# Performance work log

Measured on AMD Instinct MI355X. Metric: run time of the kernel, lower is better.

The kernel has to match this reference:

```python
import jax, jax.numpy as jnp
import numpy as np

ALPHA = 1.0

def setup_inputs() -> dict:
    key = jax.random.key(0)
    k1, k2 = jax.random.split(key)
    N, K, D = 524288, 256, 256
    context = jax.random.normal(k1, (N, D), dtype=jnp.float32)
    clusters = jax.random.normal(k2, (K, D), dtype=jnp.float32)
    return {"context": context, "clusters": clusters}

def reference(context, clusters):
    # Squared euclidean distance via the matmul trick: same math as
    # sum((x[:,None]-c)**2, -1) but avoids materializing (N,K,D).
    x2 = jnp.sum(context * context, axis=1, keepdims=True)          # (N,1)
    c2 = jnp.sum(clusters * clusters, axis=1)                       # (K,)
    xc = context @ clusters.T                                       # (N,K)
    distance = x2 + c2 - 2.0 * xc                                   # (N,K)
    q = 1.0 / (1.0 + distance / ALPHA)
    q = q ** ((ALPHA + 1.0) / 2.0)
    q = q / jnp.sum(q, axis=1, keepdims=True)                        # row-normalize
    return q
```

## Files before the change

kernel.cpp:

```cpp
#include <hip/hip_runtime.h>
#include <hip/hip_bf16.h>


#define DD 256
#define KC 256
#define BM 64
#define NT 2

typedef __attribute__((ext_vector_type(4)))  float f32x4;
typedef __attribute__((ext_vector_type(16))) float f32x16;
typedef __attribute__((ext_vector_type(8)))  short bf16x8;
typedef __attribute__((ext_vector_type(4)))  short bf16x4;
typedef __attribute__((ext_vector_type(4)))  unsigned u32x4;

__device__ __forceinline__ short f2bf(float f) {
    union { float f; unsigned u; } v; v.f = f;
    unsigned r = (v.u + 0x7fffu + ((v.u >> 16) & 1u)) >> 16;
    return (short)r;
}

__device__ __forceinline__ float bf2f(short h) {
    return __builtin_bit_cast(float, ((unsigned)(unsigned short)h) << 16);
}

__device__ __forceinline__ unsigned cvtpk(float a, float b) {
    unsigned r;
    asm("v_cvt_pk_bf16_f32 %0, %1, %2" : "=v"(r) : "v"(a), "v"(b));
    return r;
}

__device__ __forceinline__ float frcp(float x) {
    return __builtin_amdgcn_rcpf(x);
}

template<int CTRL>
__device__ __forceinline__ float dpp_add(float v) {
    int iv = __builtin_bit_cast(int, v);
    int mv = __builtin_amdgcn_update_dpp(0, iv, CTRL, 0xf, 0xf, false);
    return v + __builtin_bit_cast(float, mv);
}
#define QUAD_SWAP1 0xB1

__device__ __forceinline__ f32x4 ld4(const float* p) { return *(const f32x4*)p; }

__global__ __launch_bounds__(64)
void prep_clusters(const float* __restrict__ clus, short* __restrict__ wsb) {
    const int c = blockIdx.x;
    const int t = threadIdx.x;
    f32x4 v = *(const f32x4*)(clus + c * DD + t * 4);
    bf16x4 o;
    o[0] = f2bf(-2.f * v[0]); o[1] = f2bf(-2.f * v[1]);
    o[2] = f2bf(-2.f * v[2]); o[3] = f2bf(-2.f * v[3]);

    const int j    = t >> 1;
    const int ks   = j >> 1;
    const int hi   = j & 1;
    const int half = t & 1;
    const int nj   = c >> 5;
    const int l31  = c & 31;
    *(bf16x4*)&wsb[(((nj * 17 + ks) * 64 + hi * 32 + l31) << 3) + half * 4] = o;

    float s = v[0]*v[0] + v[1]*v[1] + v[2]*v[2] + v[3]*v[3];
    s += __shfl_xor(s, 1);  s += __shfl_xor(s, 2);  s += __shfl_xor(s, 4);
    s += __shfl_xor(s, 8);  s += __shfl_xor(s, 16); s += __shfl_xor(s, 32);
    if (t == 0) {
        float e = 1.f + s;
        short h = f2bf(e);  float e1 = e - bf2f(h);
        short m = f2bf(e1); float e2 = e1 - bf2f(m);
        short l = f2bf(e2);
        u32x4 a;
        a[0] = (unsigned)(unsigned short)h | ((unsigned)(unsigned short)m << 16);
        a[1] = (unsigned)(unsigned short)l;
        a[2] = 0u; a[3] = 0u;
        *(u32x4*)&wsb[((nj * 17 + 16) * 64 + l31) * 8] = a;
        u32x4 z = {0u, 0u, 0u, 0u};
        *(u32x4*)&wsb[((nj * 17 + 16) * 64 + 32 + l31) * 8] = z;
    }
}

__device__ __forceinline__ void convert_tile(const f32x4* u, short* AfB,
                                             float (*x2p)[64], int w, int lane) {
    const int r0   = lane >> 1;
    const int half = lane & 1;
#pragma unroll
    for (int m = 0; m < 2; ++m) {
        float xs = 0.f;
#pragma unroll
        for (int c = 0; c < 2; ++c) {
            f32x4 a0 = u[m * 4 + 2 * c], a1 = u[m * 4 + 2 * c + 1];
            u32x4 o;
            o[0] = cvtpk(a0[0], a0[1]);
            o[1] = cvtpk(a0[2], a0[3]);
            o[2] = cvtpk(a1[0], a1[1]);
            o[3] = cvtpk(a1[2], a1[3]);
            xs += a0[0]*a0[0] + a0[1]*a0[1] + a0[2]*a0[2] + a0[3]*a0[3]
                + a1[0]*a1[0] + a1[1]*a1[1] + a1[2]*a1[2] + a1[3]*a1[3];
            const int j = w * 4 + half * 2 + c;
            *(u32x4*)&AfB[(j * 64 + m * 32 + r0) * 8] = o;
        }
        xs = dpp_add<QUAD_SWAP1>(xs);
        if (half == 0) x2p[w][m * 32 + r0] = xs;
    }
}

__global__ __launch_bounds__(512, 4)
void cluster_q_main(const float* __restrict__ ctx,
                    const short* __restrict__ wsb,
                    float* __restrict__ out) {
    __shared__ short Af[NT][32 * 64 * 8];
    __shared__ float x2p8[NT][8][64];
    __shared__ float rowsum2[8][2][64];

    const int t    = threadIdx.x;
    const int lane = t & 63;
    const int w    = t >> 6;
    const int l31  = lane & 31;
    const int hi   = lane >> 5;
    const size_t row_blk = (size_t)blockIdx.x * (BM * NT);

    const int r0   = lane >> 1;
    const int half = lane & 1;
    const float* src0 = ctx + (row_blk + (size_t)r0) * DD + w * 32 + half * 16;

    f32x4 u[8];

#pragma unroll
    for (int jj = 0; jj < 8; ++jj)
        u[jj] = ld4(src0 + (size_t)((jj >> 2) * 32) * DD + (jj & 3) * 4);
    convert_tile(u, &Af[0][0], x2p8[0], w, lane);
    __syncthreads();

    const short* bl = wsb + (size_t)(w * 17) * 512 + lane * 8;

    bf16x8 ctx_aug = (bf16x8)0;
    if (hi == 0) {
        ctx_aug[0] = (short)0x3F80; ctx_aug[1] = (short)0x3F80;
        ctx_aug[2] = (short)0x3F80;
    }

#pragma unroll
    for (int tile = 0; tile < NT; ++tile) {
        const size_t trow = row_blk + (size_t)tile * BM;

        float x2A = 0.f, x2B = 0.f;
#pragma unroll
        for (int q = 0; q < 8; ++q) {
            x2A += x2p8[tile][q][l31];
            x2B += x2p8[tile][q][32 + l31];
        }

        f32x16 acc0 = (f32x16)0.f, acc1 = (f32x16)0.f;

        bf16x8 bs[3];
        bs[0] = *(const bf16x8*)(bl + 0 * 512);
        bs[1] = *(const bf16x8*)(bl + 1 * 512);
        bf16x8 bsa = *(const bf16x8*)(bl + 16 * 512);

        const short* AfC = &Af[tile][0];
        bf16x8 afA0 = *(const bf16x8*)&AfC[((0 + hi) * 64 +  0 + l31) * 8];
        bf16x8 afA1 = *(const bf16x8*)&AfC[((0 + hi) * 64 + 32 + l31) * 8];
        bf16x8 afB0, afB1;

#pragma unroll
        for (int ks = 0; ks < 16; ++ks) {
            const int cur = ks % 3;
            const bool even = (ks & 1) == 0;

            if (ks < 14)
                bs[(ks + 2) % 3] = *(const bf16x8*)(bl + (ks + 2) * 512);
            if (ks < 15) {
                const int jn = (ks + 1) * 2 + hi;
                bf16x8 v0 = *(const bf16x8*)&AfC[(jn * 64 +  0 + l31) * 8];
                bf16x8 v1 = *(const bf16x8*)&AfC[(jn * 64 + 32 + l31) * 8];
                if (even) { afB0 = v0; afB1 = v1; }
                else      { afA0 = v0; afA1 = v1; }
            }
            if (tile + 1 < NT && (ks & 3) == 0) {
                const int j0 = (ks >> 2) * 2;
#pragma unroll
                for (int jj = 0; jj < 2; ++jj) {
                    const int jx = j0 + jj;
                    u[jx] = ld4(src0 + (size_t)(BM + (jx >> 2) * 32) * DD
                                     + (jx & 3) * 4);
                }
            }

            const bf16x8 a0 = even ? afA0 : afB0;
            const bf16x8 a1 = even ? afA1 : afB1;
            acc0 = __builtin_amdgcn_mfma_f32_32x32x16_bf16(bs[cur], a0, acc0, 0, 0, 0);
            acc1 = __builtin_amdgcn_mfma_f32_32x32x16_bf16(bs[cur], a1, acc1, 0, 0, 0);
        }

        acc0 = __builtin_amdgcn_mfma_f32_32x32x16_bf16(bsa, ctx_aug, acc0, 0, 0, 0);
        acc1 = __builtin_amdgcn_mfma_f32_32x32x16_bf16(bsa, ctx_aug, acc1, 0, 0, 0);

        float s0 = 0.f, s1 = 0.f;
#pragma unroll
        for (int r = 0; r < 16; ++r) {
            acc0[r] = frcp(acc0[r] + x2A); s0 += acc0[r];
            acc1[r] = frcp(acc1[r] + x2B); s1 += acc1[r];
        }
        rowsum2[w][hi][l31]      = s0;
        rowsum2[w][hi][32 + l31] = s1;
        __syncthreads();

        float t0 = 0.f, t1 = 0.f;
#pragma unroll
        for (int q = 0; q < 8; ++q) {
            t0 += rowsum2[q][0][l31]      + rowsum2[q][1][l31];
            t1 += rowsum2[q][0][32 + l31] + rowsum2[q][1][32 + l31];
        }
        const float inv0 = frcp(t0);
        const float inv1 = frcp(t1);

        float* op0 = out + (trow + (size_t)l31) * KC        + w * 32 + 4 * hi;
        float* op1 = out + (trow + (size_t)(32 + l31)) * KC + w * 32 + 4 * hi;
#pragma unroll
        for (int i = 0; i < 4; ++i) {
            f32x4 v0, v1;
#pragma unroll
            for (int j = 0; j < 4; ++j) {
                v0[j] = acc0[4 * i + j] * inv0;
                v1[j] = acc1[4 * i + j] * inv1;
            }
            *(f32x4*)(op0 + 8 * i) = v0;
            *(f32x4*)(op1 + 8 * i) = v1;
        }

        if (tile + 1 < NT) {
            convert_tile(u, &Af[tile + 1][0], x2p8[tile + 1], w, lane);
            __syncthreads();
        }
    }
}

extern "C" void kernel_launch(void* const* d_in, const int* in_sizes, int n_in,
                              void* d_out, int out_size, void* d_ws, size_t ws_size,
                              hipStream_t stream) {
    const float* ctx  = (const float*)d_in[0];
    const float* clus = (const float*)d_in[1];
    float* out = (float*)d_out;

    short* wsb = (short*)d_ws;

    const int nrows = in_sizes[0] / DD;
    const int grid  = nrows / (BM * NT);

    hipLaunchKernelGGL(prep_clusters, dim3(KC), dim3(64), 0, stream, clus, wsb);
    hipLaunchKernelGGL(cluster_q_main, dim3(grid), dim3(512), 0, stream,
                       ctx, wsb, out);
}
```

Measured before the change: 251.4 us.

## Stream K-chunks of a single 64-row tile through double-buffered LDS

Each block now handles one 64-row tile instead of two. The tile's context is loaded in four 64-wide K chunks into a two-slot LDS buffer, and the next chunk is converted while MFMAs run on the current one. This shrinks LDS use, and launch bounds rise to allow 6 blocks per CU, aiming for more occupancy and overlap of global loads with compute. The cost is extra __syncthreads per K chunk and a grid twice as large.

```diff
diff --git a/kernel.cpp b/kernel.cpp
--- a/kernel.cpp
+++ b/kernel.cpp
@@ -5,7 +5,6 @@
 #define DD 256
 #define KC 256
 #define BM 64
-#define NT 2
 
 typedef __attribute__((ext_vector_type(4)))  float f32x4;
 typedef __attribute__((ext_vector_type(16))) float f32x16;
@@ -32,14 +31,6 @@
 __device__ __forceinline__ float frcp(float x) {
     return __builtin_amdgcn_rcpf(x);
 }
-
-template<int CTRL>
-__device__ __forceinline__ float dpp_add(float v) {
-    int iv = __builtin_bit_cast(int, v);
-    int mv = __builtin_amdgcn_update_dpp(0, iv, CTRL, 0xf, 0xf, false);
-    return v + __builtin_bit_cast(float, mv);
-}
-#define QUAD_SWAP1 0xB1
 
 __device__ __forceinline__ f32x4 ld4(const float* p) { return *(const f32x4*)p; }
 
@@ -78,37 +69,12 @@
     }
 }
 
-__device__ __forceinline__ void convert_tile(const f32x4* u, short* AfB,
-                                             float (*x2p)[64], int w, int lane) {
-    const int r0   = lane >> 1;
-    const int half = lane & 1;
-#pragma unroll
-    for (int m = 0; m < 2; ++m) {
-        float xs = 0.f;
-#pragma unroll
-        for (int c = 0; c < 2; ++c) {
-            f32x4 a0 = u[m * 4 + 2 * c], a1 = u[m * 4 + 2 * c + 1];
-            u32x4 o;
-            o[0] = cvtpk(a0[0], a0[1]);
-            o[1] = cvtpk(a0[2], a0[3]);
-            o[2] = cvtpk(a1[0], a1[1]);
-            o[3] = cvtpk(a1[2], a1[3]);
-            xs += a0[0]*a0[0] + a0[1]*a0[1] + a0[2]*a0[2] + a0[3]*a0[3]
-                + a1[0]*a1[0] + a1[1]*a1[1] + a1[2]*a1[2] + a1[3]*a1[3];
-            const int j = w * 4 + half * 2 + c;
-            *(u32x4*)&AfB[(j * 64 + m * 32 + r0) * 8] = o;
-        }
-        xs = dpp_add<QUAD_SWAP1>(xs);
-        if (half == 0) x2p[w][m * 32 + r0] = xs;
-    }
-}
-
-__global__ __launch_bounds__(512, 4)
+__global__ __launch_bounds__(512, 6)
 void cluster_q_main(const float* __restrict__ ctx,
                     const short* __restrict__ wsb,
                     float* __restrict__ out) {
-    __shared__ short Af[NT][32 * 64 * 8];
-    __shared__ float x2p8[NT][8][64];
+    __shared__ short Af[2][8 * 64 * 8];
+    __shared__ float x2row[64];
     __shared__ float rowsum2[8][2][64];
 
     const int t    = threadIdx.x;
@@ -116,121 +82,140 @@
     const int w    = t >> 6;
     const int l31  = lane & 31;
     const int hi   = lane >> 5;
-    const size_t row_blk = (size_t)blockIdx.x * (BM * NT);
-
-    const int r0   = lane >> 1;
-    const int half = lane & 1;
-    const float* src0 = ctx + (row_blk + (size_t)r0) * DD + w * 32 + half * 16;
-
-    f32x4 u[8];
-
-#pragma unroll
-    for (int jj = 0; jj < 8; ++jj)
-        u[jj] = ld4(src0 + (size_t)((jj >> 2) * 32) * DD + (jj & 3) * 4);
-    convert_tile(u, &Af[0][0], x2p8[0], w, lane);
+    const size_t row0 = (size_t)blockIdx.x * BM;
+
+    const int srow = t >> 3;
+    const int soct = t & 7;
+    const float* src = ctx + (row0 + (size_t)srow) * DD + soct * 8;
+
+    const short* bl = wsb + (size_t)(w * 17) * 512 + lane * 8;
+
+    f32x4 ua[2], ub[2];
+    ua[0] = ld4(src);        ub[0] = ld4(src + 4);
+    ua[1] = ld4(src + 64);   ub[1] = ld4(src + 68);
+
+    float xs = 0.f;
+
+    {
+        f32x4 a0 = ua[0], a1 = ub[0];
+        u32x4 o;
+        o[0] = cvtpk(a0[0], a0[1]); o[1] = cvtpk(a0[2], a0[3]);
+        o[2] = cvtpk(a1[0], a1[1]); o[3] = cvtpk(a1[2], a1[3]);
+        xs += a0[0]*a0[0] + a0[1]*a0[1] + a0[2]*a0[2] + a0[3]*a0[3]
+            + a1[0]*a1[0] + a1[1]*a1[1] + a1[2]*a1[2] + a1[3]*a1[3];
+        *(u32x4*)&Af[0][(soct * 64 + srow) * 8] = o;
+    }
     __syncthreads();
 
-    const short* bl = wsb + (size_t)(w * 17) * 512 + lane * 8;
-
-    bf16x8 ctx_aug = (bf16x8)0;
-    if (hi == 0) {
-        ctx_aug[0] = (short)0x3F80; ctx_aug[1] = (short)0x3F80;
-        ctx_aug[2] = (short)0x3F80;
-    }
-
-#pragma unroll
-    for (int tile = 0; tile < NT; ++tile) {
-        const size_t trow = row_blk + (size_t)tile * BM;
-
-        float x2A = 0.f, x2B = 0.f;
-#pragma unroll
-        for (int q = 0; q < 8; ++q) {
-            x2A += x2p8[tile][q][l31];
-            x2B += x2p8[tile][q][32 + l31];
-        }
-
-        f32x16 acc0 = (f32x16)0.f, acc1 = (f32x16)0.f;
-
-        bf16x8 bs[3];
-        bs[0] = *(const bf16x8*)(bl + 0 * 512);
-        bs[1] = *(const bf16x8*)(bl + 1 * 512);
-        bf16x8 bsa = *(const bf16x8*)(bl + 16 * 512);
-
-        const short* AfC = &Af[tile][0];
-        bf16x8 afA0 = *(const bf16x8*)&AfC[((0 + hi) * 64 +  0 + l31) * 8];
-        bf16x8 afA1 = *(const bf16x8*)&AfC[((0 + hi) * 64 + 32 + l31) * 8];
-        bf16x8 afB0, afB1;
-
-#pragma unroll
-        for (int ks = 0; ks < 16; ++ks) {
-            const int cur = ks % 3;
-            const bool even = (ks & 1) == 0;
-
-            if (ks < 14)
-                bs[(ks + 2) % 3] = *(const bf16x8*)(bl + (ks + 2) * 512);
-            if (ks < 15) {
-                const int jn = (ks + 1) * 2 + hi;
-                bf16x8 v0 = *(const bf16x8*)&AfC[(jn * 64 +  0 + l31) * 8];
+    f32x16 acc0 = (f32x16)0.f, acc1 = (f32x16)0.f;
+
+    bf16x8 bs[2];
+    bs[0] = *(const bf16x8*)(bl);
+
+    bf16x8 afA0 = *(const bf16x8*)&Af[0][(hi * 64 + l31) * 8];
+    bf16x8 afA1 = *(const bf16x8*)&Af[0][(hi * 64 + 32 + l31) * 8];
+    bf16x8 afB0, afB1;
+
+#pragma unroll
+    for (int kc = 0; kc < 4; ++kc) {
+        const int buf = kc & 1;
+        const short* AfC = &Af[buf][0];
+        const short* AfN = &Af[buf ^ 1][0];
+
+        if (kc < 2) {
+            ua[buf] = ld4(src + (kc + 2) * 64);
+            ub[buf] = ld4(src + (kc + 2) * 64 + 4);
+        }
+
+#pragma unroll
+        for (int s = 0; s < 4; ++s) {
+            const int gs = kc * 4 + s;
+
+            if (gs < 15)
+                bs[(gs + 1) & 1] = *(const bf16x8*)(bl + (gs + 1) * 512);
+
+            if (s < 3) {
+                const int jn = (s + 1) * 2 + hi;
+                bf16x8 v0 = *(const bf16x8*)&AfC[(jn * 64 + l31) * 8];
                 bf16x8 v1 = *(const bf16x8*)&AfC[(jn * 64 + 32 + l31) * 8];
-                if (even) { afB0 = v0; afB1 = v1; }
-                else      { afA0 = v0; afA1 = v1; }
+                if (s & 1) { afA0 = v0; afA1 = v1; }
+                else       { afB0 = v0; afB1 = v1; }
             }
-            if (tile + 1 < NT && (ks & 3) == 0) {
-                const int j0 = (ks >> 2) * 2;
-#pragma unroll
-                for (int jj = 0; jj < 2; ++jj) {
-                    const int jx = j0 + jj;
-                    u[jx] = ld4(src0 + (size_t)(BM + (jx >> 2) * 32) * DD
-                                     + (jx & 3) * 4);
+
+            const bf16x8 a0 = (s & 1) ? afB0 : afA0;
+            const bf16x8 a1 = (s & 1) ? afB1 : afA1;
+            acc0 = __builtin_amdgcn_mfma_f32_32x32x16_bf16(bs[gs & 1], a0, acc0, 0, 0, 0);
+            acc1 = __builtin_amdgcn_mfma_f32_32x32x16_bf16(bs[gs & 1], a1, acc1, 0, 0, 0);
+
+            if (s == 1 && kc < 3) {
+                f32x4 c0 = ua[buf ^ 1], c1 = ub[buf ^ 1];
+                u32x4 o;
+                o[0] = cvtpk(c0[0], c0[1]); o[1] = cvtpk(c0[2], c0[3]);
+                o[2] = cvtpk(c1[0], c1[1]); o[3] = cvtpk(c1[2], c1[3]);
+                xs += c0[0]*c0[0] + c0[1]*c0[1] + c0[2]*c0[2] + c0[3]*c0[3]
+                    + c1[0]*c1[0] + c1[1]*c1[1] + c1[2]*c1[2] + c1[3]*c1[3];
+                *(u32x4*)&Af[buf ^ 1][(soct * 64 + srow) * 8] = o;
+                if (kc == 2) {
+                    float xr = xs;
+                    xr += __shfl_xor(xr, 1);
+                    xr += __shfl_xor(xr, 2);
+                    xr += __shfl_xor(xr, 4);
+                    if ((lane & 7) == 0) x2row[srow] = xr;
                 }
             }
-
-            const bf16x8 a0 = even ? afA0 : afB0;
-            const bf16x8 a1 = even ? afA1 : afB1;
-            acc0 = __builtin_amdgcn_mfma_f32_32x32x16_bf16(bs[cur], a0, acc0, 0, 0, 0);
-            acc1 = __builtin_amdgcn_mfma_f32_32x32x16_bf16(bs[cur], a1, acc1, 0, 0, 0);
-        }
-
+        }
+
+        if (kc < 3) {
+            __syncthreads();
+            afA0 = *(const bf16x8*)&AfN[(hi * 64 + l31) * 8];
+            afA1 = *(const bf16x8*)&AfN[(hi * 64 + 32 + l31) * 8];
+        }
+    }
+
+    {
+        bf16x8 bsa = *(const bf16x8*)(bl + 16 * 512);
+        bf16x8 ctx_aug = (bf16x8)0;
+        if (hi == 0) {
+            ctx_aug[0] = (short)0x3F80; ctx_aug[1] = (short)0x3F80;
+            ctx_aug[2] = (short)0x3F80;
+        }
         acc0 = __builtin_amdgcn_mfma_f32_32x32x16_bf16(bsa, ctx_aug, acc0, 0, 0, 0);
         acc1 = __builtin_amdgcn_mfma_f32_32x32x16_bf16(bsa, ctx_aug, acc1, 0, 0, 0);
-
-        float s0 = 0.f, s1 = 0.f;
-#pragma unroll
-        for (int r = 0; r < 16; ++r) {
-            acc0[r] = frcp(acc0[r] + x2A); s0 += acc0[r];
-            acc1[r] = frcp(acc1[r] + x2B); s1 += acc1[r];
-        }
-        rowsum2[w][hi][l31]      = s0;
-        rowsum2[w][hi][32 + l31] = s1;
-        __syncthreads();
-
-        float t0 = 0.f, t1 = 0.f;
-#pragma unroll
-        for (int q = 0; q < 8; ++q) {
-            t0 += rowsum2[q][0][l31]      + rowsum2[q][1][l31];
-            t1 += rowsum2[q][0][32 + l31] + rowsum2[q][1][32 + l31];
-        }
-        const float inv0 = frcp(t0);
-        const float inv1 = frcp(t1);
-
-        float* op0 = out + (trow + (size_t)l31) * KC        + w * 32 + 4 * hi;
-        float* op1 = out + (trow + (size_t)(32 + l31)) * KC + w * 32 + 4 * hi;
-#pragma unroll
-        for (int i = 0; i < 4; ++i) {
-            f32x4 v0, v1;
-#pragma unroll
-            for (int j = 0; j < 4; ++j) {
-                v0[j] = acc0[4 * i + j] * inv0;
-                v1[j] = acc1[4 * i + j] * inv1;
-            }
-            *(f32x4*)(op0 + 8 * i) = v0;
-            *(f32x4*)(op1 + 8 * i) = v1;
-        }
-
-        if (tile + 1 < NT) {
-            convert_tile(u, &Af[tile + 1][0], x2p8[tile + 1], w, lane);
-            __syncthreads();
-        }
+    }
+
+    const float x2A = x2row[l31];
+    const float x2B = x2row[32 + l31];
+    float s0 = 0.f, s1 = 0.f;
+#pragma unroll
+    for (int r = 0; r < 16; ++r) {
+        acc0[r] = frcp(acc0[r] + x2A); s0 += acc0[r];
+        acc1[r] = frcp(acc1[r] + x2B); s1 += acc1[r];
+    }
+    rowsum2[w][hi][l31]      = s0;
+    rowsum2[w][hi][32 + l31] = s1;
+    __syncthreads();
+
+    float t0 = 0.f, t1 = 0.f;
+#pragma unroll
+    for (int q = 0; q < 8; ++q) {
+        t0 += rowsum2[q][0][l31]      + rowsum2[q][1][l31];
+        t1 += rowsum2[q][0][32 + l31] + rowsum2[q][1][32 + l31];
+    }
+    const float inv0 = frcp(t0);
+    const float inv1 = frcp(t1);
+
+    float* op0 = out + (row0 + (size_t)l31) * KC        + w * 32 + 4 * hi;
+    float* op1 = out + (row0 + (size_t)(32 + l31)) * KC + w * 32 + 4 * hi;
+#pragma unroll
+    for (int i = 0; i < 4; ++i) {
+        f32x4 v0, v1;
+#pragma unroll
+        for (int j = 0; j < 4; ++j) {
+            v0[j] = acc0[4 * i + j] * inv0;
+            v1[j] = acc1[4 * i + j] * inv1;
+        }
+        *(f32x4*)(op0 + 8 * i) = v0;
+        *(f32x4*)(op1 + 8 * i) = v1;
     }
 }
 
@@ -244,7 +229,7 @@
     short* wsb = (short*)d_ws;
 
     const int nrows = in_sizes[0] / DD;
-    const int grid  = nrows / (BM * NT);
+    const int grid  = nrows / BM;
 
     hipLaunchKernelGGL(prep_clusters, dim3(KC), dim3(64), 0, stream, clus, wsb);
     hipLaunchKernelGGL(cluster_q_main, dim3(grid), dim3(512), 0, stream,
```

Measured after the change: 269.7 us. +7.3%, slower.
